# Kernel optimization log

Hardware: AMD Instinct MI355X
Metric: run time of the kernel (lower is better)

## Reference

```python
import jax, jax.numpy as jnp
import numpy as np

EPS_COS = 1e-8  # torch cosine_similarity eps
EPS_LN = 1e-5   # torch LayerNorm eps


def setup_inputs() -> dict:
    key = jax.random.key(0)
    ks = jax.random.split(key, 8)
    B, N, D, C = 256, 65536, 1024, 103
    s = 1.0 / np.sqrt(D)
    return {
        "visual_input": jnp.zeros((1,), jnp.float32),
        "query_input": jax.random.normal(ks[0], (B, D), jnp.float32),
        "memory_keys": jax.random.normal(ks[1], (N, D), jnp.float32),
        "W_enc": jax.random.normal(ks[2], (D, D), jnp.float32) * s,
        "b_enc": jnp.zeros((D,), jnp.float32),
        "W_d": jax.random.normal(ks[3], (D, D), jnp.float32) * s,
        "b_d": jnp.zeros((D,), jnp.float32),
        "ln_g": jnp.ones((D,), jnp.float32),
        "ln_b": jnp.zeros((D,), jnp.float32),
        "W_cls": jax.random.normal(ks[4], (C, 2 * D), jnp.float32) * (1.0 / np.sqrt(2 * D)),
        "b_cls": jnp.zeros((C,), jnp.float32),
        "k": 32,
    }


def reference(visual_input, query_input, memory_keys, W_enc, b_enc, W_d, b_d,
              ln_g, ln_b, W_cls, b_cls, k):
    # visual encoder + relu -> query embedding [B, D]
    q = jax.nn.relu(query_input @ W_enc.T + b_enc)
    # cosine-similarity kNN over memory bank [N, D]
    qn = q / jnp.maximum(jnp.linalg.norm(q, axis=-1, keepdims=True), EPS_COS)
    mn = memory_keys / jnp.maximum(jnp.linalg.norm(memory_keys, axis=-1, keepdims=True), EPS_COS)
    sim = qn @ mn.T                      # [B, N]
    _, idx = jax.lax.top_k(sim, k)       # [B, k]
    mk = memory_keys[idx]                # [B, k, D] gather
    # memory attention
    qt = jax.nn.relu(q @ W_d.T + b_d)    # [B, D]
    scores = jnp.einsum('bd,bkd->bk', qt, mk)
    w = jax.nn.softmax(scores, axis=-1)
    attended = jnp.einsum('bk,bkd->bd', w, mk)
    x = attended + q
    mu = jnp.mean(x, axis=-1, keepdims=True)
    var = jnp.mean((x - mu) ** 2, axis=-1, keepdims=True)
    ma_out = (x - mu) * jax.lax.rsqrt(var + EPS_LN) * ln_g + ln_b
    # classifier on concatenated features
    merged = jnp.concatenate([q, ma_out], axis=1)  # [B, 2D]
    return merged @ W_cls.T + b_cls
```

## Files before the change

### kernel.cpp

```cpp
#include <hip/hip_runtime.h>
#include <stdint.h>

typedef unsigned short u16;
typedef unsigned int u32;
typedef __attribute__((ext_vector_type(2))) float f32x2;
typedef __attribute__((ext_vector_type(4))) float f32x4;
typedef __attribute__((ext_vector_type(4))) u32 u32x4;
typedef __attribute__((ext_vector_type(2))) u32 u32x2;
typedef __attribute__((ext_vector_type(8))) short bf16x8;

#define NKEYS 65536
#define DIM 1024
#define BQ 256
#define NCLS 103
#define NCAND 64
#define SROW 40

__device__ __forceinline__ u16 f2bf(float x) {
  u32 u = __float_as_uint(x);
  u = u + 0x7FFFu + ((u >> 16) & 1u);
  return (u16)(u >> 16);
}
__device__ __forceinline__ u32 cvtpk(float lo, float hi) {
  u32 d;
  asm("v_cvt_pk_bf16_f32 %0, %1, %2" : "=v"(d) : "v"(lo), "v"(hi));
  return d;
}

__global__ __launch_bounds__(256) void gemm_nt_f32(
    const float* __restrict__ A, const float* __restrict__ B,
    float* __restrict__ partial)
{
  __shared__ float sAT[16][68];
  __shared__ float sBT[16][68];
  const int tid = threadIdx.x;
  const int n0 = blockIdx.x * 64;
  const int m0 = blockIdx.y * 64;
  const int kz = blockIdx.z;
  const int r = tid & 63, kq = tid >> 6;
  const int tx = tid & 15, ty = tid >> 4;
  float acc[4][4] = {};
  for (int kb = 0; kb < 256; kb += 16) {
    const int kg = kz * 256 + kb + kq * 4;
    const f32x4 av = *(const f32x4*)(A + (size_t)(m0 + r) * DIM + kg);
    const f32x4 bv = *(const f32x4*)(B + (size_t)(n0 + r) * DIM + kg);
    __syncthreads();
#pragma unroll
    for (int i = 0; i < 4; ++i) {
      sAT[kq * 4 + i][r] = av[i];
      sBT[kq * 4 + i][r] = bv[i];
    }
    __syncthreads();
#pragma unroll
    for (int kk = 0; kk < 16; ++kk) {
      const f32x4 a4 = *(const f32x4*)&sAT[kk][ty * 4];
      const f32x4 b4 = *(const f32x4*)&sBT[kk][tx * 4];
#pragma unroll
      for (int i = 0; i < 4; ++i)
#pragma unroll
        for (int j = 0; j < 4; ++j) acc[i][j] += a4[i] * b4[j];
    }
  }
#pragma unroll
  for (int i = 0; i < 4; ++i) {
    f32x4 ov = {acc[i][0], acc[i][1], acc[i][2], acc[i][3]};
    *(f32x4*)(partial + (size_t)kz * 262144u + (size_t)(m0 + ty * 4 + i) * DIM + n0 + tx * 4) = ov;
  }
}

__global__ __launch_bounds__(256) void reduce_bias_relu(
    const float* __restrict__ partial, const float* __restrict__ bias,
    float* __restrict__ outf, u16* __restrict__ outb, const int wbf)
{
  const int i4 = blockIdx.x * 256 + threadIdx.x;
  const int e = i4 * 4;
  const int n = e & (DIM - 1);
  f32x4 s = *(const f32x4*)(partial + e);
  s += *(const f32x4*)(partial + 262144u + e);
  s += *(const f32x4*)(partial + 2u * 262144u + e);
  s += *(const f32x4*)(partial + 3u * 262144u + e);
  s += *(const f32x4*)(bias + n);
#pragma unroll
  for (int i = 0; i < 4; ++i) s[i] = fmaxf(s[i], 0.f);
  *(f32x4*)(outf + e) = s;
  if (wbf) {
    u32x2 h = {cvtpk(s[0], s[1]), cvtpk(s[2], s[3])};
    *(u32x2*)(outb + e) = h;
  }
}

__global__ __launch_bounds__(512) void simgemm(
    const float* __restrict__ keys, const u16* __restrict__ qb,
    u16* __restrict__ sim)
{
  __shared__ u16 sA[2][256 * SROW];
  __shared__ u16 sB[2][128 * SROW];
  __shared__ float snorm[128];
  const int tid = threadIdx.x;
  const int n0 = blockIdx.x * 128;

  const int a_r = tid >> 1;
  const int a_h = (tid & 1) * 16;
  const u16* agp = qb + (size_t)a_r * DIM + a_h;
  const int a_ws = a_r * SROW + a_h;

  const int b_r = tid >> 2;
  const int b_q = (tid & 3) * 8;
  const float* bgp = keys + (size_t)(n0 + b_r) * DIM + b_q;
  const int b_ws = b_r * SROW + b_q;

  const int lane = tid & 63, wave = tid >> 6;
  const int wm = (wave >> 1) * 64;
  const int wn = (wave & 1) * 64;
  const int lr = lane & 15;
  const int lk = (lane >> 4) * 8;
  const int l4 = (lane >> 4) * 4;

  float nrm = 0.f;
  f32x4 acc[4][4];
#pragma unroll
  for (int i = 0; i < 4; ++i)
#pragma unroll
    for (int j = 0; j < 4; ++j) acc[i][j] = (f32x4){0.f, 0.f, 0.f, 0.f};

  f32x4 bv0a, bv1a, bv0b, bv1b;
  u32x4 av0a, av1a, av0b, av1b;

#define LOAD_STAGE(B0, B1, A0, A1, T) do { \
    B0 = *(const f32x4*)(bgp + (size_t)(T) * 32); \
    B1 = *(const f32x4*)(bgp + (size_t)(T) * 32 + 4); \
    A0 = *(const u32x4*)(agp + (size_t)(T) * 32); \
    A1 = *(const u32x4*)(agp + (size_t)(T) * 32 + 8); \
  } while (0)

#define WRITE_STAGE(B0, B1, A0, A1, BUF) do { \
    nrm += B0[0]*B0[0] + B0[1]*B0[1] + B0[2]*B0[2] + B0[3]*B0[3]; \
    nrm += B1[0]*B1[0] + B1[1]*B1[1] + B1[2]*B1[2] + B1[3]*B1[3]; \
    u32x4 bp; \
    bp.x = cvtpk(B0[0], B0[1]); bp.y = cvtpk(B0[2], B0[3]); \
    bp.z = cvtpk(B1[0], B1[1]); bp.w = cvtpk(B1[2], B1[3]); \
    *(u32x4*)&sB[BUF][b_ws] = bp; \
    *(u32x4*)&sA[BUF][a_ws] = A0; \
    *(u32x4*)&sA[BUF][a_ws + 8] = A1; \
  } while (0)

#define COMPUTE(BUF) do { \
    bf16x8 af[4], bfr[4]; \
    _Pragma("unroll") \
    for (int f = 0; f < 4; ++f) { \
      af[f]  = *(const bf16x8*)&sA[BUF][(wm + f * 16 + lr) * SROW + lk]; \
      bfr[f] = *(const bf16x8*)&sB[BUF][(wn + f * 16 + lr) * SROW + lk]; \
    } \
    _Pragma("unroll") \
    for (int i = 0; i < 4; ++i) \
      _Pragma("unroll") \
      for (int j = 0; j < 4; ++j) \
        acc[i][j] = __builtin_amdgcn_mfma_f32_16x16x32_bf16(af[i], bfr[j], acc[i][j], 0, 0, 0); \
  } while (0)

  LOAD_STAGE(bv0a, bv1a, av0a, av1a, 0);
  WRITE_STAGE(bv0a, bv1a, av0a, av1a, 0);
  LOAD_STAGE(bv0b, bv1b, av0b, av1b, 1);
  __syncthreads();

  for (int tt = 0; tt < 32; tt += 2) {
    if (tt + 2 < 32) LOAD_STAGE(bv0a, bv1a, av0a, av1a, tt + 2);
    COMPUTE(0);
    WRITE_STAGE(bv0b, bv1b, av0b, av1b, 1);
    __syncthreads();
    if (tt + 3 < 32) LOAD_STAGE(bv0b, bv1b, av0b, av1b, tt + 3);
    COMPUTE(1);
    if (tt + 2 < 32) WRITE_STAGE(bv0a, bv1a, av0a, av1a, 0);
    __syncthreads();
  }
#undef LOAD_STAGE
#undef WRITE_STAGE
#undef COMPUTE

  nrm += __shfl_xor(nrm, 1);
  nrm += __shfl_xor(nrm, 2);
  if ((tid & 3) == 0) snorm[b_r] = nrm;
  __syncthreads();

#pragma unroll
  for (int j = 0; j < 4; ++j) {
    const int nl = wn + j * 16 + lr;
    const float scl = 1.f / fmaxf(sqrtf(snorm[nl]), 1e-8f);
    const size_t ng = (size_t)(n0 + nl);
#pragma unroll
    for (int i = 0; i < 4; ++i) {
      const int mb = wm + i * 16 + l4;
#pragma unroll
      for (int r = 0; r < 4; ++r) {
        sim[(size_t)(mb + r) * NKEYS + ng] = f2bf(acc[i][j][r] * scl);
      }
    }
  }
}

__global__ __launch_bounds__(512) void select_attn_cls(
    const u16* __restrict__ sim, const float* __restrict__ keys,
    const float* __restrict__ q, const float* __restrict__ qt,
    const float* __restrict__ ln_g, const float* __restrict__ ln_b,
    const float* __restrict__ Wc, const float* __restrict__ bc,
    float* __restrict__ out)
{
  __shared__ int redc[8];
  __shared__ int sc1, sc2;
  __shared__ int clist[NCAND];
  __shared__ float sdq[NCAND], sdqt[NCAND], snr[NCAND];
  __shared__ int srowi[32];
  __shared__ float sw[32];
  __shared__ float red1[8], red2[8];
  __shared__ float smg[2048];
  const int tid = threadIdx.x, lane = tid & 63, wave = tid >> 6;
  const int m = blockIdx.x;

  const u32x4* row = (const u32x4*)(sim + (size_t)m * NKEYS);
  u32 ku[16][4];
#pragma unroll
  for (int i = 0; i < 16; ++i) {
    const u32x4 v = row[i * 512 + tid];
#pragma unroll
    for (int c = 0; c < 4; ++c) {
      u32 lo = v[c] & 0xFFFFu, hi = v[c] >> 16;
      lo ^= (lo & 0x8000u) ? 0xFFFFu : 0x8000u;
      hi ^= (hi & 0x8000u) ? 0xFFFFu : 0x8000u;
      ku[i][c] = lo | (hi << 16);
    }
  }
  int lo_b = 0, hi_b = 65536;
  while (hi_b - lo_b > 1) {
    const u32 mid = (u32)((lo_b + hi_b) >> 1);
    int c = 0;
#pragma unroll
    for (int i = 0; i < 16; ++i)
#pragma unroll
      for (int k = 0; k < 4; ++k) {
        const u32 x = ku[i][k];
        c += ((x & 0xFFFFu) >= mid) ? 1 : 0;
        c += ((x >> 16) >= mid) ? 1 : 0;
      }
#pragma unroll
    for (int j = 32; j; j >>= 1) c += __shfl_xor(c, j);
    if ((tid & 63) == 0) redc[tid >> 6] = c;
    __syncthreads();
    int tot = 0;
#pragma unroll
    for (int w = 0; w < 8; ++w) tot += redc[w];
    if (tot >= NCAND) lo_b = (int)mid; else hi_b = (int)mid;
    __syncthreads();
  }
  const u32 tau = (u32)lo_b;

  int ch = 0;
#pragma unroll
  for (int i = 0; i < 16; ++i)
#pragma unroll
    for (int k = 0; k < 4; ++k) {
      const u32 x = ku[i][k];
      ch += ((x & 0xFFFFu) > tau) ? 1 : 0;
      ch += ((x >> 16) > tau) ? 1 : 0;
    }
#pragma unroll
  for (int j = 32; j; j >>= 1) ch += __shfl_xor(ch, j);
  if ((tid & 63) == 0) redc[tid >> 6] = ch;
  if (tid == 0) { sc1 = 0; sc2 = 0; }
  __syncthreads();
  int nhi = 0;
#pragma unroll
  for (int w = 0; w < 8; ++w) nhi += redc[w];

#pragma unroll
  for (int i = 0; i < 16; ++i)
#pragma unroll
    for (int k = 0; k < 4; ++k) {
      const int nb = (i * 512 + tid) * 8 + k * 2;
      const u32 x = ku[i][k];
      const u32 l = x & 0xFFFFu, h = x >> 16;
      if (l > tau) { int p = atomicAdd(&sc1, 1); clist[p] = nb; }
      else if (l == tau) { int p = atomicAdd(&sc2, 1); if (nhi + p < NCAND) clist[nhi + p] = nb; }
      if (h > tau) { int p = atomicAdd(&sc1, 1); clist[p] = nb + 1; }
      else if (h == tau) { int p = atomicAdd(&sc2, 1); if (nhi + p < NCAND) clist[nhi + p] = nb + 1; }
    }
  __syncthreads();

  f32x4 q4[4], qt4[4];
#pragma unroll
  for (int i = 0; i < 4; ++i) {
    q4[i]  = *(const f32x4*)(q  + (size_t)m * DIM + i * 256 + lane * 4);
    qt4[i] = *(const f32x4*)(qt + (size_t)m * DIM + i * 256 + lane * 4);
  }
  for (int ci = 0; ci < 8; ++ci) {
    const int c = wave * 8 + ci;
    const float* kr = keys + (size_t)clist[c] * DIM;
    float dq = 0.f, dt = 0.f, ss = 0.f;
#pragma unroll
    for (int i = 0; i < 4; ++i) {
      const f32x4 kv = *(const f32x4*)(kr + i * 256 + lane * 4);
#pragma unroll
      for (int e = 0; e < 4; ++e) {
        dq += kv[e] * q4[i][e];
        dt += kv[e] * qt4[i][e];
        ss += kv[e] * kv[e];
      }
    }
#pragma unroll
    for (int j = 32; j; j >>= 1) {
      dq += __shfl_xor(dq, j);
      dt += __shfl_xor(dt, j);
      ss += __shfl_xor(ss, j);
    }
    if (lane == 0) { sdq[c] = dq; sdqt[c] = dt; snr[c] = ss; }
  }
  __syncthreads();

  if (wave == 0) {
    float v = sdq[lane] / fmaxf(sqrtf(snr[lane]), 1e-8f);
    int p = lane;
#pragma unroll
    for (int k = 2; k <= 64; k <<= 1)
#pragma unroll
      for (int j = k >> 1; j > 0; j >>= 1) {
        const float ov = __shfl_xor(v, j);
        const int op = __shfl_xor(p, j);
        const bool tl = ((lane & j) == 0) == ((lane & k) == 0);
        const bool take = tl ? (ov > v) : (ov < v);
        if (take) { v = ov; p = op; }
      }
    float sc = (lane < 32) ? sdqt[p] : -3.4e38f;
    float mx = sc;
#pragma unroll
    for (int j = 16; j; j >>= 1) mx = fmaxf(mx, __shfl_xor(mx, j));
    const float e = (lane < 32) ? expf(sc - mx) : 0.f;
    float s = e;
#pragma unroll
    for (int j = 16; j; j >>= 1) s += __shfl_xor(s, j);
    if (lane < 32) { sw[lane] = e / s; srowi[lane] = clist[p]; }
  }
  __syncthreads();

  const int d0 = tid * 2;
  f32x2 at = {0.f, 0.f};
  for (int j = 0; j < 32; ++j) {
    const float wj = sw[j];
    const f32x2 kv = *(const f32x2*)(keys + (size_t)srowi[j] * DIM + d0);
    at += wj * kv;
  }
  const f32x2 qv = *(const f32x2*)(q + (size_t)m * DIM + d0);
  const f32x2 x = at + qv;
  float s1 = x[0] + x[1];
#pragma unroll
  for (int j = 32; j; j >>= 1) s1 += __shfl_xor(s1, j);
  if (lane == 0) red1[wave] = s1;
  __syncthreads();
  float mu = 0.f;
#pragma unroll
  for (int w = 0; w < 8; ++w) mu += red1[w];
  mu *= (1.f / 1024.f);
  const f32x2 xc = x - mu;
  float s2 = xc[0] * xc[0] + xc[1] * xc[1];
#pragma unroll
  for (int j = 32; j; j >>= 1) s2 += __shfl_xor(s2, j);
  if (lane == 0) red2[wave] = s2;
  __syncthreads();
  float var = 0.f;
#pragma unroll
  for (int w = 0; w < 8; ++w) var += red2[w];
  var *= (1.f / 1024.f);
  const float rstd = rsqrtf(var + 1e-5f);
  const f32x2 g = *(const f32x2*)(ln_g + d0);
  const f32x2 b = *(const f32x2*)(ln_b + d0);
  const f32x2 ma = xc * rstd * g + b;
  *(f32x2*)&smg[d0] = qv;
  *(f32x2*)&smg[1024 + d0] = ma;
  __syncthreads();

  for (int c = wave; c < NCLS; c += 8) {
    const float* w = Wc + (size_t)c * 2048;
    float a = 0.f;
#pragma unroll
    for (int i = 0; i < 8; ++i) {
      const f32x4 wv = *(const f32x4*)(w + i * 256 + lane * 4);
      const f32x4 mv = *(const f32x4*)&smg[i * 256 + lane * 4];
#pragma unroll
      for (int e = 0; e < 4; ++e) a += wv[e] * mv[e];
    }
#pragma unroll
    for (int j = 32; j; j >>= 1) a += __shfl_xor(a, j);
    if (lane == 0) out[(size_t)m * NCLS + c] = a + bc[c];
  }
}

extern "C" void kernel_launch(void* const* d_in, const int* in_sizes, int n_in,
                              void* d_out, int out_size, void* d_ws, size_t ws_size,
                              hipStream_t stream)
{
  const float* query = (const float*)d_in[1];
  const float* keys  = (const float*)d_in[2];
  const float* Wenc  = (const float*)d_in[3];
  const float* benc  = (const float*)d_in[4];
  const float* Wd    = (const float*)d_in[5];
  const float* bd    = (const float*)d_in[6];
  const float* lng   = (const float*)d_in[7];
  const float* lnb   = (const float*)d_in[8];
  const float* Wcls  = (const float*)d_in[9];
  const float* bcls  = (const float*)d_in[10];
  float* out = (float*)d_out;
  char* ws = (char*)d_ws;

  float* q   = (float*)(ws + 0);
  float* qt  = (float*)(ws + 1048576u);
  u16*   qb  = (u16*)(ws + 2097152u);
  char*  big = ws + 2621440u;
  float* par = (float*)big;
  u16*   sim = (u16*)big;

  gemm_nt_f32<<<dim3(16, 4, 4), 256, 0, stream>>>(query, Wenc, par);
  reduce_bias_relu<<<256, 256, 0, stream>>>(par, benc, q, qb, 1);
  gemm_nt_f32<<<dim3(16, 4, 4), 256, 0, stream>>>(q, Wd, par);
  reduce_bias_relu<<<256, 256, 0, stream>>>(par, bd, qt, qb, 0);
  simgemm<<<dim3(512), 512, 0, stream>>>(keys, qb, sim);
  select_attn_cls<<<256, 512, 0, stream>>>(sim, keys, q, qt, lng, lnb, Wcls, bcls, out);
}
```

Baseline: 197.7 us.

## Double-buffer fp32 GEMM smem and deepen key prefetch in similarity kernel

The fp32 split-K GEMM now uses double-buffered shared memory tiles. This removes one barrier per k-step and overlaps the global loads for the next tile with compute on the current one. The bf16 MFMA similarity kernel now prefetches the memory-key tiles four stages ahead in registers instead of two, to hide more global-load latency on the large key stream. The cost is extra registers, which may lower occupancy, and twice the LDS for the small GEMM.

```diff
diff --git a/kernel.cpp b/kernel.cpp
--- a/kernel.cpp
+++ b/kernel.cpp
@@ -31,8 +31,8 @@
     const float* __restrict__ A, const float* __restrict__ B,
     float* __restrict__ partial)
 {
-  __shared__ float sAT[16][68];
-  __shared__ float sBT[16][68];
+  __shared__ float sAT[2][16][68];
+  __shared__ float sBT[2][16][68];
   const int tid = threadIdx.x;
   const int n0 = blockIdx.x * 64;
   const int m0 = blockIdx.y * 64;
@@ -40,26 +40,42 @@
   const int r = tid & 63, kq = tid >> 6;
   const int tx = tid & 15, ty = tid >> 4;
   float acc[4][4] = {};
-  for (int kb = 0; kb < 256; kb += 16) {
-    const int kg = kz * 256 + kb + kq * 4;
-    const f32x4 av = *(const f32x4*)(A + (size_t)(m0 + r) * DIM + kg);
-    const f32x4 bv = *(const f32x4*)(B + (size_t)(n0 + r) * DIM + kg);
-    __syncthreads();
-#pragma unroll
-    for (int i = 0; i < 4; ++i) {
-      sAT[kq * 4 + i][r] = av[i];
-      sBT[kq * 4 + i][r] = bv[i];
-    }
-    __syncthreads();
+
+  const float* ag = A + (size_t)(m0 + r) * DIM + kz * 256 + kq * 4;
+  const float* bg = B + (size_t)(n0 + r) * DIM + kz * 256 + kq * 4;
+
+  f32x4 av = *(const f32x4*)(ag);
+  f32x4 bv = *(const f32x4*)(bg);
+#pragma unroll
+  for (int i = 0; i < 4; ++i) {
+    sAT[0][kq * 4 + i][r] = av[i];
+    sBT[0][kq * 4 + i][r] = bv[i];
+  }
+  __syncthreads();
+
+  for (int kb = 0; kb < 16; ++kb) {
+    const int cur = kb & 1;
+    if (kb + 1 < 16) {
+      av = *(const f32x4*)(ag + (kb + 1) * 16);
+      bv = *(const f32x4*)(bg + (kb + 1) * 16);
+    }
 #pragma unroll
     for (int kk = 0; kk < 16; ++kk) {
-      const f32x4 a4 = *(const f32x4*)&sAT[kk][ty * 4];
-      const f32x4 b4 = *(const f32x4*)&sBT[kk][tx * 4];
+      const f32x4 a4 = *(const f32x4*)&sAT[cur][kk][ty * 4];
+      const f32x4 b4 = *(const f32x4*)&sBT[cur][kk][tx * 4];
 #pragma unroll
       for (int i = 0; i < 4; ++i)
 #pragma unroll
         for (int j = 0; j < 4; ++j) acc[i][j] += a4[i] * b4[j];
     }
+    if (kb + 1 < 16) {
+#pragma unroll
+      for (int i = 0; i < 4; ++i) {
+        sAT[cur ^ 1][kq * 4 + i][r] = av[i];
+        sBT[cur ^ 1][kq * 4 + i][r] = bv[i];
+      }
+    }
+    __syncthreads();
   }
 #pragma unroll
   for (int i = 0; i < 4; ++i) {
@@ -123,17 +139,18 @@
 #pragma unroll
     for (int j = 0; j < 4; ++j) acc[i][j] = (f32x4){0.f, 0.f, 0.f, 0.f};
 
-  f32x4 bv0a, bv1a, bv0b, bv1b;
-  u32x4 av0a, av1a, av0b, av1b;
-
-#define LOAD_STAGE(B0, B1, A0, A1, T) do { \
+  f32x4 b00, b01, b10, b11, b20, b21, b30, b31;
+  u32x4 a00, a01, a10, a11;
+
+#define LOADB(B0, B1, T) do { \
     B0 = *(const f32x4*)(bgp + (size_t)(T) * 32); \
     B1 = *(const f32x4*)(bgp + (size_t)(T) * 32 + 4); \
+  } while (0)
+#define LOADA(A0, A1, T) do { \
     A0 = *(const u32x4*)(agp + (size_t)(T) * 32); \
     A1 = *(const u32x4*)(agp + (size_t)(T) * 32 + 8); \
   } while (0)
-
-#define WRITE_STAGE(B0, B1, A0, A1, BUF) do { \
+#define WRITE(B0, B1, A0, A1, BUF) do { \
     nrm += B0[0]*B0[0] + B0[1]*B0[1] + B0[2]*B0[2] + B0[3]*B0[3]; \
     nrm += B1[0]*B1[0] + B1[1]*B1[1] + B1[2]*B1[2] + B1[3]*B1[3]; \
     u32x4 bp; \
@@ -143,7 +160,6 @@
     *(u32x4*)&sA[BUF][a_ws] = A0; \
     *(u32x4*)&sA[BUF][a_ws + 8] = A1; \
   } while (0)
-
 #define COMPUTE(BUF) do { \
     bf16x8 af[4], bfr[4]; \
     _Pragma("unroll") \
@@ -158,23 +174,36 @@
         acc[i][j] = __builtin_amdgcn_mfma_f32_16x16x32_bf16(af[i], bfr[j], acc[i][j], 0, 0, 0); \
   } while (0)
 
-  LOAD_STAGE(bv0a, bv1a, av0a, av1a, 0);
-  WRITE_STAGE(bv0a, bv1a, av0a, av1a, 0);
-  LOAD_STAGE(bv0b, bv1b, av0b, av1b, 1);
-  __syncthreads();
-
-  for (int tt = 0; tt < 32; tt += 2) {
-    if (tt + 2 < 32) LOAD_STAGE(bv0a, bv1a, av0a, av1a, tt + 2);
+  LOADB(b00, b01, 0); LOADB(b10, b11, 1); LOADB(b20, b21, 2); LOADB(b30, b31, 3);
+  LOADA(a00, a01, 0); LOADA(a10, a11, 1);
+  WRITE(b00, b01, a00, a01, 0);
+  __syncthreads();
+
+  for (int tt = 0; tt < 32; tt += 4) {
+    if (tt + 4 < 32) LOADB(b00, b01, tt + 4);
+    LOADA(a00, a01, tt + 2);
     COMPUTE(0);
-    WRITE_STAGE(bv0b, bv1b, av0b, av1b, 1);
-    __syncthreads();
-    if (tt + 3 < 32) LOAD_STAGE(bv0b, bv1b, av0b, av1b, tt + 3);
+    WRITE(b10, b11, a10, a11, 1);
+    __syncthreads();
+    if (tt + 5 < 32) LOADB(b10, b11, tt + 5);
+    LOADA(a10, a11, tt + 3);
     COMPUTE(1);
-    if (tt + 2 < 32) WRITE_STAGE(bv0a, bv1a, av0a, av1a, 0);
-    __syncthreads();
-  }
-#undef LOAD_STAGE
-#undef WRITE_STAGE
+    WRITE(b20, b21, a00, a01, 0);
+    __syncthreads();
+    if (tt + 6 < 32) LOADB(b20, b21, tt + 6);
+    if (tt + 4 < 32) LOADA(a00, a01, tt + 4);
+    COMPUTE(0);
+    WRITE(b30, b31, a10, a11, 1);
+    __syncthreads();
+    if (tt + 7 < 32) LOADB(b30, b31, tt + 7);
+    if (tt + 5 < 32) LOADA(a10, a11, tt + 5);
+    COMPUTE(1);
+    if (tt + 4 < 32) WRITE(b00, b01, a00, a01, 0);
+    __syncthreads();
+  }
+#undef LOADB
+#undef LOADA
+#undef WRITE
 #undef COMPUTE
 
   nrm += __shfl_xor(nrm, 1);
```

Measured after the change: 183.5 us. 7.2% less time.
